# Kernel tuning notes

Measured on AMD Instinct MI355X. Metric: run time of the kernel, lower is better.

## Reference

```python
import jax, jax.numpy as jnp
import numpy as np
from jax import lax

B, T, F, H, NC = 64, 256, 64, 128, 2


def setup_inputs() -> dict:
    key = jax.random.key(0)
    ks = jax.random.split(key, 10)
    # timestamps: sorted ints with duplicates -> exercises per-timestamp mean aggregation
    t = jnp.sort(jax.random.randint(ks[0], (B, T), 0, T // 2), axis=1).astype(jnp.float32)
    m = jax.random.randint(ks[1], (B, T), 0, F).astype(jnp.float32)
    x = jax.random.normal(ks[2], (B, T), dtype=jnp.float32)
    delt = jax.random.uniform(ks[3], (B, T), dtype=jnp.float32)
    X = jnp.stack([t, m, x, delt], axis=1)  # [B, 4, T]
    lengths = jax.random.randint(ks[4], (B,), T // 2, T + 1).astype(jnp.int32)
    s = 1.0 / np.sqrt(H + 1)
    W_lin = jax.random.uniform(ks[5], (F, H + 1, 4 * H), minval=-s, maxval=s, dtype=jnp.float32)
    b_lin = jax.random.uniform(ks[6], (F, 4 * H), minval=-s, maxval=s, dtype=jnp.float32)
    W_dec = jax.random.uniform(ks[7], (F,), minval=-1.0, maxval=1.0, dtype=jnp.float32)
    b_dec = jax.random.uniform(ks[8], (F,), minval=-1.0, maxval=1.0, dtype=jnp.float32)
    so = 1.0 / np.sqrt(F * H + H)
    k9, k10 = jax.random.split(ks[9])
    W_out = jax.random.uniform(k9, (F * H + H, NC), minval=-so, maxval=so, dtype=jnp.float32)
    b_out = jax.random.uniform(k10, (NC,), minval=-so, maxval=so, dtype=jnp.float32)
    return {"X": X, "lengths": lengths, "W_lin": W_lin, "b_lin": b_lin,
            "W_dec": W_dec, "b_dec": b_dec, "W_out": W_out, "b_out": b_out}


def _forward(X, lengths, W_lin, b_lin, W_dec, b_dec, W_out, b_out):
    nF, Hp1, H4 = W_lin.shape
    hs = Hp1 - 1
    t = X[:, 0]
    m = X[:, 1].astype(jnp.int32)
    x = X[:, 2]
    delt = X[:, 3]
    idx = jnp.arange(t.shape[1])
    valid = idx[None, :] < lengths[:, None]                       # event is real
    t_next = jnp.concatenate([t[:, 1:], t[:, -1:] + 1.0], axis=1)
    # last event of a consecutive-equal-timestamp group (within valid length)
    boundary = (idx[None, :] == (lengths[:, None] - 1)) | (t_next != t)

    def per_sample(m_s, x_s, d_s, v_s, b_s):
        def step(carry, inp):
            h_t, c_t, acc, cnt = carry
            mj, xj, dj, vj, bj = inp
            # feature-specific decay of that feature's hidden row
            dm = W_dec[mj] * dj + b_dec[mj]
            decay = jnp.exp(-jnp.maximum(0.0, dm))
            h_dec = decay * h_t[mj]
            inp_vec = jnp.concatenate([xj[None], h_dec])          # [H+1]
            gates = inp_vec @ W_lin[mj] + b_lin[mj]               # [4H]
            gi, gf, go, gc = jnp.split(gates, 4)
            c_cand = jax.nn.sigmoid(gf) * c_t + jax.nn.sigmoid(gi) * jnp.tanh(gc)
            h_row = jax.nn.sigmoid(go) * jnp.tanh(c_cand)
            h_t = jnp.where(vj, h_t.at[mj].set(h_row), h_t)
            acc = acc + jnp.where(vj, c_cand, 0.0)
            cnt = cnt + jnp.where(vj, 1.0, 0.0)
            close = vj & bj                                       # end of timestamp group
            c_t = jnp.where(close, acc / jnp.maximum(cnt, 1.0), c_t)
            acc = jnp.where(close, jnp.zeros_like(acc), acc)
            cnt = jnp.where(close, 0.0, cnt)
            return (h_t, c_t, acc, cnt), None

        init = (jnp.zeros((nF, hs), jnp.float32), jnp.zeros((hs,), jnp.float32),
                jnp.zeros((hs,), jnp.float32), jnp.float32(0.0))
        (h_t, c_t, _, _), _ = lax.scan(step, init, (m_s, x_s, d_s, v_s, b_s))
        feats = jnp.concatenate([c_t, h_t.reshape(-1)])           # [H + F*H]
        return jax.nn.softmax(feats @ W_out + b_out)

    return jax.vmap(per_sample)(m, x, delt, valid, boundary)      # [B, n_class]


def reference(X, lengths, W_lin, b_lin, W_dec, b_dec, W_out, b_out):
    return _forward(X, lengths, W_lin, b_lin, W_dec, b_dec, W_out, b_out)
```

## Files before the change

### kernel.cpp

```cpp
#include <hip/hip_runtime.h>
#include <math.h>
#include <stdint.h>

#define BATCH 64
#define T 256
#define NF 64
#define H 128
#define H4 512
#define HP1 129
#define WF_STRIDE (HP1 * H4)
#define FEATS (NF * H + H)
#define NTH 1024

#define PACK_U4 (NF * 4 * 1024)
#define PACK_BYTES ((size_t)PACK_U4 * 16u)
#define AUX_BYTES ((size_t)NF * 1024 * 16u)
#define WS_NEED (PACK_BYTES + AUX_BYTES)

typedef float vf2 __attribute__((ext_vector_type(2)));

__device__ __forceinline__ float sigmoidf_(float x) {
    return 1.0f / (1.0f + __expf(-x));
}

__device__ __forceinline__ float tanhf_(float x) {
    float ax = fabsf(x);
    float e = __expf(2.0f * ax);
    float r = 1.0f - 2.0f / (e + 1.0f);
    return copysignf(r, x);
}

template<bool HI>
__device__ __forceinline__ vf2 dec2f(unsigned u) {
    return __builtin_amdgcn_cvt_pk_f32_fp8(u, HI);
}

__global__ __launch_bounds__(256)
void repack6_kernel(const float* __restrict__ W_lin, uint4* __restrict__ pack) {
    const int lin = blockIdx.x * 256 + threadIdx.x;
    const int t   = lin & 1023;
    const int i   = (lin >> 10) & 3;
    const int f   = lin >> 12;
    const int kq  = t >> 7;
    const int cg  = t & 127;
    const int col = i * 128 + cg;
    unsigned u[4];
    #pragma unroll
    for (int w = 0; w < 4; ++w) {
        const float* src = W_lin + (size_t)f * WF_STRIDE
                         + (size_t)(1 + kq * 16 + 4 * w) * H4 + col;
        const float v0 = src[0]      * 4096.0f;
        const float v1 = src[H4]     * 4096.0f;
        const float v2 = src[2 * H4] * 4096.0f;
        const float v3 = src[3 * H4] * 4096.0f;
        unsigned r = 0;
        r = __builtin_amdgcn_cvt_pk_fp8_f32(v0, v1, r, false);
        r = __builtin_amdgcn_cvt_pk_fp8_f32(v2, v3, r, true);
        u[w] = r;
    }
    uint4 o; o.x = u[0]; o.y = u[1]; o.z = u[2]; o.w = u[3];
    pack[lin] = o;
}

__global__ __launch_bounds__(256)
void aux6_kernel(const float* __restrict__ W_lin, const float* __restrict__ b_lin,
                 float4* __restrict__ aux) {
    const int lin = blockIdx.x * 256 + threadIdx.x;
    const int t   = lin & 1023;
    const int f   = lin >> 10;
    const int kq  = t >> 7;
    const int cg  = t & 127;
    float4 o = make_float4(0.f, 0.f, 0.f, 0.f);
    if (kq == 0) {
        o.x = W_lin[(size_t)f * WF_STRIDE + cg];
        o.y = W_lin[(size_t)f * WF_STRIDE + 128 + cg];
        o.z = W_lin[(size_t)f * WF_STRIDE + 256 + cg];
        o.w = W_lin[(size_t)f * WF_STRIDE + 384 + cg];
    } else if (kq == 1) {
        o.x = b_lin[f * H4 + cg];
        o.y = b_lin[f * H4 + 128 + cg];
        o.z = b_lin[f * H4 + 256 + cg];
        o.w = b_lin[f * H4 + 384 + cg];
    }
    aux[lin] = o;
}

__global__ __launch_bounds__(NTH, 2)
void lstm_scan_fp8_v4(const float* __restrict__ X,
                      const int* __restrict__ lengths,
                      const float* __restrict__ W_dec,
                      const float* __restrict__ b_dec,
                      const float* __restrict__ W_out,
                      const float* __restrict__ b_out,
                      const uint4* __restrict__ pack,
                      const float4* __restrict__ aux,
                      float* __restrict__ out)
{
    __shared__ float s_feats[FEATS];
    __shared__ float s_inp[H];
    __shared__ float s_part[8][H4];
    __shared__ float s_X[4 * T];
    __shared__ float s_wdec[NF];
    __shared__ float s_bdec[NF];
    __shared__ float s_red[32];

    float* s_ct = s_feats;
    float* s_ht = s_feats + H;

    const int tid = threadIdx.x;
    const int b   = blockIdx.x;
    const int cg  = tid & 127;
    const int kq  = tid >> 7;

    const float* Xb = X + b * 4 * T;
    const int len = lengths[b];

    for (int i = tid; i < NF * H; i += NTH) s_ht[i] = 0.0f;
    for (int i = tid; i < 4 * T; i += NTH) s_X[i] = Xb[i];
    if (tid < NF) { s_wdec[tid] = W_dec[tid]; s_bdec[tid] = b_dec[tid]; }
    if (tid < H) s_inp[tid] = 0.0f;
    __syncthreads();

    float c_t = 0.0f, accs = 0.0f, cnts = 0.0f;

    #define DOTC(W, ACC) do {                                                   \
        vf2 d;                                                                  \
        d = dec2f<false>((W).x); ACC += d * iv8[0];                             \
        d = dec2f<true >((W).x); ACC += d * iv8[1];                             \
        d = dec2f<false>((W).y); ACC += d * iv8[2];                             \
        d = dec2f<true >((W).y); ACC += d * iv8[3];                             \
        d = dec2f<false>((W).z); ACC += d * iv8[4];                             \
        d = dec2f<true >((W).z); ACC += d * iv8[5];                             \
        d = dec2f<false>((W).w); ACC += d * iv8[6];                             \
        d = dec2f<true >((W).w); ACC += d * iv8[7];                             \
    } while (0)

    uint4 A0, A1, A2, A3, B0, B1, B2, B3;
    float4 AX = make_float4(0.f, 0.f, 0.f, 0.f), BX = AX;

    {
        const int m0 = (int)s_X[T];
        const uint4* p0 = pack + (size_t)m0 * 4096 + tid;
        A0 = p0[0]; A1 = p0[1024]; A2 = p0[2048]; A3 = p0[3072];
        AX = aux[(size_t)m0 * 1024 + tid];
    }

    #define STEP(C0, C1, C2, C3, CX, N0, N1, N2, N3, NX)                        \
    {                                                                           \
        const int   mj  = (int)s_X[T + j];                                      \
        const float xj  = s_X[2 * T + j];                                       \
        const int   jn  = (j + 1 < T) ? (j + 1) : (T - 1);                      \
        const int   mjn = (int)s_X[T + jn];                                     \
                              \
        {                                                                       \
            const uint4* pn = pack + (size_t)mjn * 4096 + tid;                  \
            N0 = pn[0]; N1 = pn[1024]; N2 = pn[2048]; N3 = pn[3072];            \
            NX = aux[(size_t)mjn * 1024 + tid];                                 \
        }                                                                       \
           \
        vf2 iv8[8];                                                             \
        {                                                                       \
            const float4* ip = (const float4*)(s_inp + kq * 16);                \
            _Pragma("unroll")                                                   \
            for (int q = 0; q < 4; ++q) {                                       \
                const float4 t_ = ip[q];                                        \
                iv8[2 * q][0] = t_.x;     iv8[2 * q][1] = t_.y;                 \
                iv8[2 * q + 1][0] = t_.z; iv8[2 * q + 1][1] = t_.w;             \
            }                                                                   \
        }                                                                       \
        vf2 ac0, ac1, ac2, ac3;                                                 \
        ac0 = 0.0f; ac1 = 0.0f; ac2 = 0.0f; ac3 = 0.0f;                         \
        DOTC(C0, ac0); DOTC(C1, ac1); DOTC(C2, ac2); DOTC(C3, ac3);             \
        float a0 = (ac0[0] + ac0[1]) * (1.0f / 4096.0f);                        \
        float a1 = (ac1[0] + ac1[1]) * (1.0f / 4096.0f);                        \
        float a2 = (ac2[0] + ac2[1]) * (1.0f / 4096.0f);                        \
        float a3 = (ac3[0] + ac3[1]) * (1.0f / 4096.0f);                        \
        if (kq == 0) {                                                          \
            a0 = fmaf(xj, CX.x, a0); a1 = fmaf(xj, CX.y, a1);                   \
            a2 = fmaf(xj, CX.z, a2); a3 = fmaf(xj, CX.w, a3);                   \
        } else if (kq == 1) {                                                   \
            a0 += CX.x; a1 += CX.y; a2 += CX.z; a3 += CX.w;                     \
        }                                                                       \
        s_part[kq][cg]       = a0;                                              \
        s_part[kq][128 + cg] = a1;                                              \
        s_part[kq][256 + cg] = a2;                                              \
        s_part[kq][384 + cg] = a3;                                              \
        __syncthreads();                                 \
        if (tid < H) {                                                          \
            const int h = tid;                                                  \
            float g0 = 0.f, g1 = 0.f, g2 = 0.f, g3 = 0.f;                       \
            _Pragma("unroll")                                                   \
            for (int q = 0; q < 8; ++q) {                                       \
                g0 += s_part[q][h];                                             \
                g1 += s_part[q][128 + h];                                       \
                g2 += s_part[q][256 + h];                                       \
                g3 += s_part[q][384 + h];                                       \
            }                                                                   \
            const float c_cand = sigmoidf_(g1) * c_t + sigmoidf_(g0) * tanhf_(g3); \
            const float h_row  = sigmoidf_(g2) * tanhf_(c_cand);                \
            s_ht[mj * H + h] = h_row;                                           \
            accs += c_cand;                                                     \
            cnts += 1.0f;                                                       \
            const float tj = s_X[j];                                            \
            const float tn = (j < T - 1) ? s_X[j + 1] : (tj + 1.0f);            \
            const bool boundary = (j == len - 1) || (tn != tj);                 \
            if (boundary) { c_t = accs / fmaxf(cnts, 1.0f); accs = 0.0f; cnts = 0.0f; } \
            const float dn  = s_X[3 * T + jn];                                  \
            const float dmn = fmaf(s_wdec[mjn], dn, s_bdec[mjn]);               \
            const float den = __expf(-fmaxf(0.0f, dmn));                        \
            const float hv  = (mjn == mj) ? h_row : s_ht[mjn * H + h];          \
            s_inp[h] = den * hv;                                                \
        }                                                                       \
        __syncthreads();                              \
    }

    int j = 0;
    while (j < len) {
        STEP(A0, A1, A2, A3, AX, B0, B1, B2, B3, BX); ++j;
        if (j >= len) break;
        STEP(B0, B1, B2, B3, BX, A0, A1, A2, A3, AX); ++j;
    }
    #undef STEP
    #undef DOTC

    if (tid < H) s_ct[tid] = c_t;
    __syncthreads();

    float z0 = 0.0f, z1 = 0.0f;
    for (int i = tid; i < FEATS; i += NTH) {
        const float f = s_feats[i];
        const float2 w = *(const float2*)(W_out + 2 * i);
        z0 = fmaf(f, w.x, z0);
        z1 = fmaf(f, w.y, z1);
    }
    #pragma unroll
    for (int off = 32; off > 0; off >>= 1) {
        z0 += __shfl_down(z0, off, 64);
        z1 += __shfl_down(z1, off, 64);
    }
    const int wave = tid >> 6, lane = tid & 63;
    if (lane == 0) { s_red[2 * wave] = z0; s_red[2 * wave + 1] = z1; }
    __syncthreads();
    if (tid == 0) {
        float a0 = b_out[0], a1 = b_out[1];
        #pragma unroll
        for (int w = 0; w < 16; ++w) { a0 += s_red[2 * w]; a1 += s_red[2 * w + 1]; }
        const float mx = fmaxf(a0, a1);
        const float e0 = __expf(a0 - mx), e1 = __expf(a1 - mx);
        const float inv = 1.0f / (e0 + e1);
        out[2 * b]     = e0 * inv;
        out[2 * b + 1] = e1 * inv;
    }
}

#define NTHREADS 512
__global__ __launch_bounds__(NTHREADS)
void lstm_scan_kernel(const float* __restrict__ X,
                      const int* __restrict__ lengths,
                      const float* __restrict__ W_lin,
                      const float* __restrict__ b_lin,
                      const float* __restrict__ W_dec,
                      const float* __restrict__ b_dec,
                      const float* __restrict__ W_out,
                      const float* __restrict__ b_out,
                      float* __restrict__ out)
{
    __shared__ float s_feats[FEATS];
    __shared__ float s_inp[H];
    __shared__ float s_part[4][H4];
    __shared__ float s_X[4 * T];
    __shared__ float s_wdec[NF];
    __shared__ float s_bdec[NF];
    __shared__ float s_red[16];

    float* s_ct = s_feats;
    float* s_ht = s_feats + H;

    const int tid = threadIdx.x;
    const int b   = blockIdx.x;
    const int g4  = tid & 127;
    const int kq  = tid >> 7;

    const float* Xb = X + b * 4 * T;
    const int len = lengths[b];

    for (int i = tid; i < NF * H; i += NTHREADS) s_ht[i] = 0.0f;
    for (int i = tid; i < 4 * T; i += NTHREADS) s_X[i] = Xb[i];
    if (tid < NF) { s_wdec[tid] = W_dec[tid]; s_bdec[tid] = b_dec[tid]; }
    __syncthreads();

    float c_t = 0.0f, acc = 0.0f, cnt = 0.0f;

    for (int j = 0; j < len; ++j) {
        const int   mj = (int)s_X[T + j];
        const float xj = s_X[2 * T + j];
        const float* Wf = W_lin + mj * WF_STRIDE;

        float bl0, bl1, bl2, bl3;
        if (tid < H) {
            const float dj    = s_X[3 * T + j];
            const float dm    = fmaf(s_wdec[mj], dj, s_bdec[mj]);
            const float decay = __expf(-fmaxf(0.0f, dm));
            s_inp[tid] = decay * s_ht[mj * H + tid];
            const int m4 = mj * H4;
            bl0 = b_lin[m4 + tid];
            bl1 = b_lin[m4 + H + tid];
            bl2 = b_lin[m4 + 2 * H + tid];
            bl3 = b_lin[m4 + 3 * H + tid];
        }
        __syncthreads();

        float4 a4 = make_float4(0.0f, 0.0f, 0.0f, 0.0f);
        {
            const float*  wr  = Wf + (1 + kq * 32) * H4 + 4 * g4;
            const float4* ivp = (const float4*)(s_inp + kq * 32);
            #pragma unroll
            for (int cc = 0; cc < 8; ++cc) {
                const float4 v = ivp[cc];
                const float* wrc = wr + (4 * cc) * H4;
                const float4 w0 = *(const float4*)(wrc);
                const float4 w1 = *(const float4*)(wrc + H4);
                const float4 w2 = *(const float4*)(wrc + 2 * H4);
                const float4 w3 = *(const float4*)(wrc + 3 * H4);
                a4.x = fmaf(v.x, w0.x, a4.x); a4.y = fmaf(v.x, w0.y, a4.y);
                a4.z = fmaf(v.x, w0.z, a4.z); a4.w = fmaf(v.x, w0.w, a4.w);
                a4.x = fmaf(v.y, w1.x, a4.x); a4.y = fmaf(v.y, w1.y, a4.y);
                a4.z = fmaf(v.y, w1.z, a4.z); a4.w = fmaf(v.y, w1.w, a4.w);
                a4.x = fmaf(v.z, w2.x, a4.x); a4.y = fmaf(v.z, w2.y, a4.y);
                a4.z = fmaf(v.z, w2.z, a4.z); a4.w = fmaf(v.z, w2.w, a4.w);
                a4.x = fmaf(v.w, w3.x, a4.x); a4.y = fmaf(v.w, w3.y, a4.y);
                a4.z = fmaf(v.w, w3.z, a4.z); a4.w = fmaf(v.w, w3.w, a4.w);
            }
        }
        if (kq == 0) {
            const float4 wv = *(const float4*)(Wf + 4 * g4);
            a4.x = fmaf(xj, wv.x, a4.x); a4.y = fmaf(xj, wv.y, a4.y);
            a4.z = fmaf(xj, wv.z, a4.z); a4.w = fmaf(xj, wv.w, a4.w);
        }
        *(float4*)(&s_part[kq][4 * g4]) = a4;
        __syncthreads();

        if (tid < H) {
            const int h = tid;
            const float gi = s_part[0][h]         + s_part[1][h]         + s_part[2][h]         + s_part[3][h]         + bl0;
            const float gf = s_part[0][H + h]     + s_part[1][H + h]     + s_part[2][H + h]     + s_part[3][H + h]     + bl1;
            const float go = s_part[0][2*H + h]   + s_part[1][2*H + h]   + s_part[2][2*H + h]   + s_part[3][2*H + h]   + bl2;
            const float gc = s_part[0][3*H + h]   + s_part[1][3*H + h]   + s_part[2][3*H + h]   + s_part[3][3*H + h]   + bl3;

            const float c_cand = sigmoidf_(gf) * c_t + sigmoidf_(gi) * tanhf_(gc);
            const float h_row  = sigmoidf_(go) * tanhf_(c_cand);
            s_ht[mj * H + h] = h_row;
            acc += c_cand;
            cnt += 1.0f;

            const float tj = s_X[j];
            const float tn = (j < T - 1) ? s_X[j + 1] : (tj + 1.0f);
            const bool boundary = (j == len - 1) || (tn != tj);
            if (boundary) { c_t = acc / fmaxf(cnt, 1.0f); acc = 0.0f; cnt = 0.0f; }
        }
        __syncthreads();
    }

    if (tid < H) s_ct[tid] = c_t;
    __syncthreads();

    float z0 = 0.0f, z1 = 0.0f;
    for (int i = tid; i < FEATS; i += NTHREADS) {
        const float f = s_feats[i];
        const float2 wv = *(const float2*)(W_out + 2 * i);
        z0 = fmaf(f, wv.x, z0);
        z1 = fmaf(f, wv.y, z1);
    }
    #pragma unroll
    for (int off = 32; off > 0; off >>= 1) {
        z0 += __shfl_down(z0, off, 64);
        z1 += __shfl_down(z1, off, 64);
    }
    const int wave = tid >> 6, lane = tid & 63;
    if (lane == 0) { s_red[2 * wave] = z0; s_red[2 * wave + 1] = z1; }
    __syncthreads();
    if (tid == 0) {
        float a0 = b_out[0], a1 = b_out[1];
        #pragma unroll
        for (int q = 0; q < 8; ++q) { a0 += s_red[2 * q]; a1 += s_red[2 * q + 1]; }
        const float mx = fmaxf(a0, a1);
        const float e0 = __expf(a0 - mx), e1 = __expf(a1 - mx);
        const float inv = 1.0f / (e0 + e1);
        out[2 * b]     = e0 * inv;
        out[2 * b + 1] = e1 * inv;
    }
}

extern "C" void kernel_launch(void* const* d_in, const int* in_sizes, int n_in,
                              void* d_out, int out_size, void* d_ws, size_t ws_size,
                              hipStream_t stream) {
    const float* X      = (const float*)d_in[0];
    const int*   lens   = (const int*)d_in[1];
    const float* W_lin  = (const float*)d_in[2];
    const float* b_lin  = (const float*)d_in[3];
    const float* W_dec  = (const float*)d_in[4];
    const float* b_dec  = (const float*)d_in[5];
    const float* W_out  = (const float*)d_in[6];
    const float* b_out  = (const float*)d_in[7];
    float* out = (float*)d_out;

    if (ws_size >= WS_NEED) {
        uint4*  pack = (uint4*)d_ws;
        float4* aux  = (float4*)((char*)d_ws + PACK_BYTES);
        hipLaunchKernelGGL(repack6_kernel, dim3(PACK_U4 / 256), dim3(256), 0, stream,
                           W_lin, pack);
        hipLaunchKernelGGL(aux6_kernel, dim3(NF * 1024 / 256), dim3(256), 0, stream,
                           W_lin, b_lin, aux);
        hipLaunchKernelGGL(lstm_scan_fp8_v4, dim3(BATCH), dim3(NTH), 0, stream,
                           X, lens, W_dec, b_dec, W_out, b_out, pack, aux, out);
    } else {
        hipLaunchKernelGGL(lstm_scan_kernel, dim3(BATCH), dim3(NTHREADS), 0, stream,
                           X, lens, W_lin, b_lin, W_dec, b_dec, W_out, b_out, out);
    }
}
```

Before: 448.7 us.

## Process two batch samples per block with 512 threads each and deeper K slices

Each 1024-thread block now runs two independent samples, 512 threads each, and launches 32 blocks instead of 64. Every thread now covers 32 K rows instead of 16, so the weight repack layout changes to 8 uint4 per thread and the partial-sum reduction drops from 8 to 4 slices. The goal is to cut the cross-thread reduction and the shared-memory traffic per step, and to run two sequences through one barrier chain. In exchange, each block loops to the longer of its two lengths, uses twice the registers per thread for weights, and the GPU runs only 32 blocks, which lowers parallelism across CUs.

```diff
diff --git a/kernel.cpp b/kernel.cpp
--- a/kernel.cpp
+++ b/kernel.cpp
@@ -12,10 +12,10 @@
 #define FEATS (NF * H + H)
 #define NTH 1024
 
-#define PACK_U4 (NF * 4 * 1024)
-#define PACK_BYTES ((size_t)PACK_U4 * 16u)
-#define AUX_BYTES ((size_t)NF * 1024 * 16u)
-#define WS_NEED (PACK_BYTES + AUX_BYTES)
+#define PACK7_U4 (NF * 8 * 512)
+#define PACK7_BYTES ((size_t)PACK7_U4 * 16u)
+#define AUX7_BYTES ((size_t)NF * 512 * 16u)
+#define WS_NEED (PACK7_BYTES + AUX7_BYTES)
 
 typedef float vf2 __attribute__((ext_vector_type(2)));
 
@@ -36,19 +36,22 @@
 }
 
 __global__ __launch_bounds__(256)
-void repack6_kernel(const float* __restrict__ W_lin, uint4* __restrict__ pack) {
+void repack7_kernel(const float* __restrict__ W_lin, uint4* __restrict__ pack) {
     const int lin = blockIdx.x * 256 + threadIdx.x;
-    const int t   = lin & 1023;
-    const int i   = (lin >> 10) & 3;
+    const int t   = lin & 511;
+    const int u   = (lin >> 9) & 7;
     const int f   = lin >> 12;
+    const int g   = u >> 1;
+    const int q   = u & 1;
     const int kq  = t >> 7;
     const int cg  = t & 127;
-    const int col = i * 128 + cg;
-    unsigned u[4];
+    const int col = g * 128 + cg;
+    const int k0  = kq * 32 + q * 16;
+    unsigned uw[4];
     #pragma unroll
     for (int w = 0; w < 4; ++w) {
         const float* src = W_lin + (size_t)f * WF_STRIDE
-                         + (size_t)(1 + kq * 16 + 4 * w) * H4 + col;
+                         + (size_t)(1 + k0 + 4 * w) * H4 + col;
         const float v0 = src[0]      * 4096.0f;
         const float v1 = src[H4]     * 4096.0f;
         const float v2 = src[2 * H4] * 4096.0f;
@@ -56,18 +59,18 @@
         unsigned r = 0;
         r = __builtin_amdgcn_cvt_pk_fp8_f32(v0, v1, r, false);
         r = __builtin_amdgcn_cvt_pk_fp8_f32(v2, v3, r, true);
-        u[w] = r;
-    }
-    uint4 o; o.x = u[0]; o.y = u[1]; o.z = u[2]; o.w = u[3];
+        uw[w] = r;
+    }
+    uint4 o; o.x = uw[0]; o.y = uw[1]; o.z = uw[2]; o.w = uw[3];
     pack[lin] = o;
 }
 
 __global__ __launch_bounds__(256)
-void aux6_kernel(const float* __restrict__ W_lin, const float* __restrict__ b_lin,
+void aux7_kernel(const float* __restrict__ W_lin, const float* __restrict__ b_lin,
                  float4* __restrict__ aux) {
     const int lin = blockIdx.x * 256 + threadIdx.x;
-    const int t   = lin & 1023;
-    const int f   = lin >> 10;
+    const int t   = lin & 511;
+    const int f   = lin >> 9;
     const int kq  = t >> 7;
     const int cg  = t & 127;
     float4 o = make_float4(0.f, 0.f, 0.f, 0.f);
@@ -85,8 +88,8 @@
     aux[lin] = o;
 }
 
-__global__ __launch_bounds__(NTH, 2)
-void lstm_scan_fp8_v4(const float* __restrict__ X,
+__global__ __launch_bounds__(NTH, 1)
+void lstm_scan_fp8_v5(const float* __restrict__ X,
                       const int* __restrict__ lengths,
                       const float* __restrict__ W_dec,
                       const float* __restrict__ b_dec,
@@ -96,139 +99,157 @@
                       const float4* __restrict__ aux,
                       float* __restrict__ out)
 {
-    __shared__ float s_feats[FEATS];
-    __shared__ float s_inp[H];
-    __shared__ float s_part[8][H4];
-    __shared__ float s_X[4 * T];
+    __shared__ float s_ht[2][NF * H];
+    __shared__ float s_inp[2][H];
+    __shared__ float s_part[2][4][H4];
+    __shared__ float s_X[2][4 * T];
     __shared__ float s_wdec[NF];
     __shared__ float s_bdec[NF];
+    __shared__ float s_cfin[2][H];
     __shared__ float s_red[32];
 
-    float* s_ct = s_feats;
-    float* s_ht = s_feats + H;
-
-    const int tid = threadIdx.x;
-    const int b   = blockIdx.x;
-    const int cg  = tid & 127;
-    const int kq  = tid >> 7;
-
-    const float* Xb = X + b * 4 * T;
-    const int len = lengths[b];
-
-    for (int i = tid; i < NF * H; i += NTH) s_ht[i] = 0.0f;
-    for (int i = tid; i < 4 * T; i += NTH) s_X[i] = Xb[i];
+    const int tid  = threadIdx.x;
+    const int blk  = blockIdx.x;
+    const int half = tid >> 9;
+    const int t    = tid & 511;
+    const int cg   = t & 127;
+    const int kq   = t >> 7;
+
+    const int bA = blk, bB = blk + 32;
+    const int myB = half ? bB : bA;
+
+    const int lenA = lengths[bA];
+    const int lenB = lengths[bB];
+    const int myLen = half ? lenB : lenA;
+    const int lenM = (lenA > lenB) ? lenA : lenB;
+
+    for (int i = tid; i < 4 * T; i += NTH) {
+        s_X[0][i] = X[bA * 4 * T + i];
+        s_X[1][i] = X[bB * 4 * T + i];
+    }
+    for (int i = tid; i < NF * H; i += NTH) { s_ht[0][i] = 0.0f; s_ht[1][i] = 0.0f; }
     if (tid < NF) { s_wdec[tid] = W_dec[tid]; s_bdec[tid] = b_dec[tid]; }
-    if (tid < H) s_inp[tid] = 0.0f;
-    __syncthreads();
+    if (tid < H) { s_inp[0][tid] = 0.0f; s_inp[1][tid] = 0.0f; }
+    __syncthreads();
+
+    const float* myX = s_X[half];
 
     float c_t = 0.0f, accs = 0.0f, cnts = 0.0f;
 
-    #define DOTC(W, ACC) do {                                                   \
+    #define DOT2(WA, WB, OUTV) do {                                             \
+        vf2 ac; ac[0] = 0.0f; ac[1] = 0.0f;                                     \
         vf2 d;                                                                  \
-        d = dec2f<false>((W).x); ACC += d * iv8[0];                             \
-        d = dec2f<true >((W).x); ACC += d * iv8[1];                             \
-        d = dec2f<false>((W).y); ACC += d * iv8[2];                             \
-        d = dec2f<true >((W).y); ACC += d * iv8[3];                             \
-        d = dec2f<false>((W).z); ACC += d * iv8[4];                             \
-        d = dec2f<true >((W).z); ACC += d * iv8[5];                             \
-        d = dec2f<false>((W).w); ACC += d * iv8[6];                             \
-        d = dec2f<true >((W).w); ACC += d * iv8[7];                             \
+        d = dec2f<false>((WA).x); ac += d * iv[0];                              \
+        d = dec2f<true >((WA).x); ac += d * iv[1];                              \
+        d = dec2f<false>((WA).y); ac += d * iv[2];                              \
+        d = dec2f<true >((WA).y); ac += d * iv[3];                              \
+        d = dec2f<false>((WA).z); ac += d * iv[4];                              \
+        d = dec2f<true >((WA).z); ac += d * iv[5];                              \
+        d = dec2f<false>((WA).w); ac += d * iv[6];                              \
+        d = dec2f<true >((WA).w); ac += d * iv[7];                              \
+        d = dec2f<false>((WB).x); ac += d * iv[8];                              \
+        d = dec2f<true >((WB).x); ac += d * iv[9];                              \
+        d = dec2f<false>((WB).y); ac += d * iv[10];                             \
+        d = dec2f<true >((WB).y); ac += d * iv[11];                             \
+        d = dec2f<false>((WB).z); ac += d * iv[12];                             \
+        d = dec2f<true >((WB).z); ac += d * iv[13];                             \
+        d = dec2f<false>((WB).w); ac += d * iv[14];                             \
+        d = dec2f<true >((WB).w); ac += d * iv[15];                             \
+        OUTV = (ac[0] + ac[1]) * (1.0f / 4096.0f);                              \
     } while (0)
 
-    uint4 A0, A1, A2, A3, B0, B1, B2, B3;
+    uint4 A0, A1, A2, A3, A4, A5, A6, A7;
+    uint4 B0, B1, B2, B3, B4, B5, B6, B7;
     float4 AX = make_float4(0.f, 0.f, 0.f, 0.f), BX = AX;
 
     {
-        const int m0 = (int)s_X[T];
-        const uint4* p0 = pack + (size_t)m0 * 4096 + tid;
-        A0 = p0[0]; A1 = p0[1024]; A2 = p0[2048]; A3 = p0[3072];
-        AX = aux[(size_t)m0 * 1024 + tid];
-    }
-
-    #define STEP(C0, C1, C2, C3, CX, N0, N1, N2, N3, NX)                        \
+        const int m0 = (int)myX[T];
+        const uint4* p0 = pack + (size_t)m0 * 4096 + t;
+        A0 = p0[0];    A1 = p0[512];  A2 = p0[1024]; A3 = p0[1536];
+        A4 = p0[2048]; A5 = p0[2560]; A6 = p0[3072]; A7 = p0[3584];
+        AX = aux[(size_t)m0 * 512 + t];
+    }
+
+    #define STEP(C0,C1,C2,C3,C4,C5,C6,C7,CX, N0,N1,N2,N3,N4,N5,N6,N7,NX)        \
     {                                                                           \
-        const int   mj  = (int)s_X[T + j];                                      \
-        const float xj  = s_X[2 * T + j];                                       \
+        const int   mj  = (int)myX[T + j];                                      \
+        const float xj  = myX[2 * T + j];                                       \
         const int   jn  = (j + 1 < T) ? (j + 1) : (T - 1);                      \
-        const int   mjn = (int)s_X[T + jn];                                     \
+        const int   mjn = (int)myX[T + jn];                                     \
                               \
         {                                                                       \
-            const uint4* pn = pack + (size_t)mjn * 4096 + tid;                  \
-            N0 = pn[0]; N1 = pn[1024]; N2 = pn[2048]; N3 = pn[3072];            \
-            NX = aux[(size_t)mjn * 1024 + tid];                                 \
+            const uint4* pn = pack + (size_t)mjn * 4096 + t;                    \
+            N0 = pn[0];    N1 = pn[512];  N2 = pn[1024]; N3 = pn[1536];         \
+            N4 = pn[2048]; N5 = pn[2560]; N6 = pn[3072]; N7 = pn[3584];         \
+            NX = aux[(size_t)mjn * 512 + t];                                    \
         }                                                                       \
-           \
-        vf2 iv8[8];                                                             \
+              \
+        vf2 iv[16];                                                             \
         {                                                                       \
-            const float4* ip = (const float4*)(s_inp + kq * 16);                \
+            const float4* ip = (const float4*)(s_inp[half] + kq * 32);          \
             _Pragma("unroll")                                                   \
-            for (int q = 0; q < 4; ++q) {                                       \
+            for (int q = 0; q < 8; ++q) {                                       \
                 const float4 t_ = ip[q];                                        \
-                iv8[2 * q][0] = t_.x;     iv8[2 * q][1] = t_.y;                 \
-                iv8[2 * q + 1][0] = t_.z; iv8[2 * q + 1][1] = t_.w;             \
+                iv[2 * q][0] = t_.x;     iv[2 * q][1] = t_.y;                   \
+                iv[2 * q + 1][0] = t_.z; iv[2 * q + 1][1] = t_.w;               \
             }                                                                   \
         }                                                                       \
-        vf2 ac0, ac1, ac2, ac3;                                                 \
-        ac0 = 0.0f; ac1 = 0.0f; ac2 = 0.0f; ac3 = 0.0f;                         \
-        DOTC(C0, ac0); DOTC(C1, ac1); DOTC(C2, ac2); DOTC(C3, ac3);             \
-        float a0 = (ac0[0] + ac0[1]) * (1.0f / 4096.0f);                        \
-        float a1 = (ac1[0] + ac1[1]) * (1.0f / 4096.0f);                        \
-        float a2 = (ac2[0] + ac2[1]) * (1.0f / 4096.0f);                        \
-        float a3 = (ac3[0] + ac3[1]) * (1.0f / 4096.0f);                        \
+        float a0, a1, a2, a3;                                                   \
+        DOT2(C0, C1, a0); DOT2(C2, C3, a1); DOT2(C4, C5, a2); DOT2(C6, C7, a3); \
         if (kq == 0) {                                                          \
             a0 = fmaf(xj, CX.x, a0); a1 = fmaf(xj, CX.y, a1);                   \
             a2 = fmaf(xj, CX.z, a2); a3 = fmaf(xj, CX.w, a3);                   \
         } else if (kq == 1) {                                                   \
             a0 += CX.x; a1 += CX.y; a2 += CX.z; a3 += CX.w;                     \
         }                                                                       \
-        s_part[kq][cg]       = a0;                                              \
-        s_part[kq][128 + cg] = a1;                                              \
-        s_part[kq][256 + cg] = a2;                                              \
-        s_part[kq][384 + cg] = a3;                                              \
+        s_part[half][kq][cg]       = a0;                                        \
+        s_part[half][kq][128 + cg] = a1;                                        \
+        s_part[half][kq][256 + cg] = a2;                                        \
+        s_part[half][kq][384 + cg] = a3;                                        \
         __syncthreads();                                 \
-        if (tid < H) {                                                          \
-            const int h = tid;                                                  \
+        if (t < H && j < myLen) {                                               \
+            const int h = t;                                                    \
             float g0 = 0.f, g1 = 0.f, g2 = 0.f, g3 = 0.f;                       \
             _Pragma("unroll")                                                   \
-            for (int q = 0; q < 8; ++q) {                                       \
-                g0 += s_part[q][h];                                             \
-                g1 += s_part[q][128 + h];                                       \
-                g2 += s_part[q][256 + h];                                       \
-                g3 += s_part[q][384 + h];                                       \
+            for (int q = 0; q < 4; ++q) {                                       \
+                g0 += s_part[half][q][h];                                       \
+                g1 += s_part[half][q][128 + h];                                 \
+                g2 += s_part[half][q][256 + h];                                 \
+                g3 += s_part[half][q][384 + h];                                 \
             }                                                                   \
             const float c_cand = sigmoidf_(g1) * c_t + sigmoidf_(g0) * tanhf_(g3); \
             const float h_row  = sigmoidf_(g2) * tanhf_(c_cand);                \
-            s_ht[mj * H + h] = h_row;                                           \
+            s_ht[half][mj * H + h] = h_row;                                     \
             accs += c_cand;                                                     \
             cnts += 1.0f;                                                       \
-            const float tj = s_X[j];                                            \
-            const float tn = (j < T - 1) ? s_X[j + 1] : (tj + 1.0f);            \
-            const bool boundary = (j == len - 1) || (tn != tj);                 \
+            const float tj = myX[j];                                            \
+            const float tn = (j < T - 1) ? myX[j + 1] : (tj + 1.0f);            \
+            const bool boundary = (j == myLen - 1) || (tn != tj);               \
             if (boundary) { c_t = accs / fmaxf(cnts, 1.0f); accs = 0.0f; cnts = 0.0f; } \
-            const float dn  = s_X[3 * T + jn];                                  \
+            const float dn  = myX[3 * T + jn];                                  \
             const float dmn = fmaf(s_wdec[mjn], dn, s_bdec[mjn]);               \
             const float den = __expf(-fmaxf(0.0f, dmn));                        \
-            const float hv  = (mjn == mj) ? h_row : s_ht[mjn * H + h];          \
-            s_inp[h] = den * hv;                                                \
+            const float hv  = (mjn == mj) ? h_row : s_ht[half][mjn * H + h];    \
+            s_inp[half][h] = den * hv;                                          \
         }                                                                       \
         __syncthreads();                              \
     }
 
     int j = 0;
-    while (j < len) {
-        STEP(A0, A1, A2, A3, AX, B0, B1, B2, B3, BX); ++j;
-        if (j >= len) break;
-        STEP(B0, B1, B2, B3, BX, A0, A1, A2, A3, AX); ++j;
+    while (j < lenM) {
+        STEP(A0,A1,A2,A3,A4,A5,A6,A7,AX, B0,B1,B2,B3,B4,B5,B6,B7,BX); ++j;
+        if (j >= lenM) break;
+        STEP(B0,B1,B2,B3,B4,B5,B6,B7,BX, A0,A1,A2,A3,A4,A5,A6,A7,AX); ++j;
     }
     #undef STEP
-    #undef DOTC
-
-    if (tid < H) s_ct[tid] = c_t;
+    #undef DOT2
+
+    if (t < H) s_cfin[half][t] = c_t;
     __syncthreads();
 
     float z0 = 0.0f, z1 = 0.0f;
-    for (int i = tid; i < FEATS; i += NTH) {
-        const float f = s_feats[i];
+    for (int i = t; i < FEATS; i += 512) {
+        const float f = (i < H) ? s_cfin[half][i] : s_ht[half][i - H];
         const float2 w = *(const float2*)(W_out + 2 * i);
         z0 = fmaf(f, w.x, z0);
         z1 = fmaf(f, w.y, z1);
@@ -241,15 +262,16 @@
     const int wave = tid >> 6, lane = tid & 63;
     if (lane == 0) { s_red[2 * wave] = z0; s_red[2 * wave + 1] = z1; }
     __syncthreads();
-    if (tid == 0) {
+    if (t == 0) {
+        const int w0 = half * 8;
         float a0 = b_out[0], a1 = b_out[1];
         #pragma unroll
-        for (int w = 0; w < 16; ++w) { a0 += s_red[2 * w]; a1 += s_red[2 * w + 1]; }
+        for (int w = 0; w < 8; ++w) { a0 += s_red[2 * (w0 + w)]; a1 += s_red[2 * (w0 + w) + 1]; }
         const float mx = fmaxf(a0, a1);
         const float e0 = __expf(a0 - mx), e1 = __expf(a1 - mx);
         const float inv = 1.0f / (e0 + e1);
-        out[2 * b]     = e0 * inv;
-        out[2 * b + 1] = e1 * inv;
+        out[2 * myB]     = e0 * inv;
+        out[2 * myB + 1] = e1 * inv;
     }
 }
 
@@ -406,12 +428,12 @@
 
     if (ws_size >= WS_NEED) {
         uint4*  pack = (uint4*)d_ws;
-        float4* aux  = (float4*)((char*)d_ws + PACK_BYTES);
-        hipLaunchKernelGGL(repack6_kernel, dim3(PACK_U4 / 256), dim3(256), 0, stream,
+        float4* aux  = (float4*)((char*)d_ws + PACK7_BYTES);
+        hipLaunchKernelGGL(repack7_kernel, dim3(PACK7_U4 / 256), dim3(256), 0, stream,
                            W_lin, pack);
-        hipLaunchKernelGGL(aux6_kernel, dim3(NF * 1024 / 256), dim3(256), 0, stream,
+        hipLaunchKernelGGL(aux7_kernel, dim3(NF * 512 / 256), dim3(256), 0, stream,
                            W_lin, b_lin, aux);
-        hipLaunchKernelGGL(lstm_scan_fp8_v4, dim3(BATCH), dim3(NTH), 0, stream,
+        hipLaunchKernelGGL(lstm_scan_fp8_v5, dim3(BATCH / 2), dim3(NTH), 0, stream,
                            X, lens, W_dec, b_dec, W_out, b_out, pack, aux, out);
     } else {
         hipLaunchKernelGGL(lstm_scan_kernel, dim3(BATCH), dim3(NTHREADS), 0, stream,
```

Measured after the change: 734.4 us. +63.7%, slower.
